# Performance work log

Hardware: AMD Instinct MI355X
Metric: run time of the kernel (lower is better)

Reference implementation:

```python
import jax, jax.numpy as jnp
import numpy as np

N, E, C, RB, H = 10000, 160000, 64, 8, 64
AVG_NEIGH = 16.0


def _sph(v):
    # component-normalized real spherical harmonics l=1,2,3 of unit vectors v [E,3]
    x, y, z = v[..., 0], v[..., 1], v[..., 2]
    s3, s5, s15 = 3.0 ** 0.5, 5.0 ** 0.5, 15.0 ** 0.5
    y1 = s3 * jnp.stack([x, y, z], -1)  # [E,3]
    y2 = jnp.stack([
        s15 * x * y,
        s15 * y * z,
        0.5 * s5 * (3.0 * z * z - 1.0),
        s15 * x * z,
        0.5 * s15 * (x * x - y * y),
    ], -1)  # [E,5]
    c1 = (35.0 / 8.0) ** 0.5
    c2 = 105.0 ** 0.5
    c3 = (21.0 / 8.0) ** 0.5
    c4 = (7.0 ** 0.5) / 2.0
    y3 = jnp.stack([
        c1 * y * (3.0 * x * x - y * y),
        c2 * x * y * z,
        c3 * y * (5.0 * z * z - 1.0),
        c4 * z * (5.0 * z * z - 3.0),
        c3 * x * (5.0 * z * z - 1.0),
        0.5 * c2 * z * (x * x - y * y),
        c1 * x * (x * x - y * y),
    ], -1)  # [E,7]
    return y1, y2, y3


def setup_inputs() -> dict:
    key = jax.random.key(0)
    ks = jax.random.split(key, 12)
    inp = {
        'vectors': jax.random.normal(ks[0], (E, 3), jnp.float32),
        'node_feats': jax.random.normal(ks[1], (N, C), jnp.float32),
        'radial_embedding': jax.random.normal(ks[2], (E, RB), jnp.float32),
        'W_up': jax.random.normal(ks[3], (C, C), jnp.float32) / np.sqrt(C),
        'mlp_w1': jax.random.normal(ks[4], (RB, H), jnp.float32) / np.sqrt(RB),
        'mlp_w2': jax.random.normal(ks[5], (H, H), jnp.float32) / np.sqrt(H),
        'mlp_w3': jax.random.normal(ks[6], (H, H), jnp.float32) / np.sqrt(H),
        'mlp_w4': jax.random.normal(ks[7], (H, 4 * C), jnp.float32) / np.sqrt(H),
        'W_down': jax.random.normal(ks[8], (4, C, C), jnp.float32) / np.sqrt(C),
        'senders': jax.random.randint(ks[9], (E,), 0, N, jnp.int32),
        'receivers': jax.random.randint(ks[10], (E,), 0, N, jnp.int32),
    }
    return inp


def reference(vectors, node_feats, radial_embedding, W_up, mlp_w1, mlp_w2, mlp_w3, mlp_w4, W_down, senders, receivers):
    n = node_feats.shape[0]
    # linear_up (scalars: plain channel mixing)
    x = node_feats @ W_up                                   # [N,C]
    sf = x[senders]                                         # [E,C] gather
    u = vectors / (jnp.linalg.norm(vectors, axis=-1, keepdims=True) + 1e-12)
    y1, y2, y3 = _sph(u)
    # radial MLP -> per-irrep mixing weights [E, 4C]
    h = jax.nn.silu(radial_embedding @ mlp_w1)
    h = jax.nn.silu(h @ mlp_w2)
    h = jax.nn.silu(h @ mlp_w3)
    mix = h @ mlp_w4
    m0, m1, m2, m3 = jnp.split(mix, 4, axis=-1)             # each [E,C]
    # tensor product of Cx0e with Y_l -> Cx(l), scaled by radial mix
    msg0 = sf * m0                                          # [E,C]
    msg1 = (sf * m1)[:, :, None] * y1[:, None, :]           # [E,C,3]
    msg2 = (sf * m2)[:, :, None] * y2[:, None, :]           # [E,C,5]
    msg3 = (sf * m3)[:, :, None] * y3[:, None, :]           # [E,C,7]
    inv = 1.0 / jnp.sqrt(jnp.asarray(AVG_NEIGH, msg0.dtype))
    seg = lambda m: jax.ops.segment_sum(m, receivers, num_segments=n) * inv
    o0, o1, o2, o3 = seg(msg0), seg(msg1), seg(msg2), seg(msg3)
    # linear_down: per-l channel mixing
    o0 = o0 @ W_down[0]
    o1 = jnp.einsum('ncm,cd->ndm', o1, W_down[1])
    o2 = jnp.einsum('ncm,cd->ndm', o2, W_down[2])
    o3 = jnp.einsum('ncm,cd->ndm', o3, W_down[3])
    return jnp.concatenate([o0, o1.reshape(n, -1), o2.reshape(n, -1), o3.reshape(n, -1)], axis=-1)  # [N, 16C]
```

## Files before the change

kernel.cpp:

```cpp
#include <hip/hip_runtime.h>
#include <math.h>

#define CC 64
typedef _Float16 f16;
typedef _Float16 half8_t __attribute__((ext_vector_type(8)));
typedef float f32x4 __attribute__((ext_vector_type(4)));

__device__ __forceinline__ float silu_f(float v) {
    return v / (1.0f + __expf(-v));
}

__global__ void k_up(const float* __restrict__ nf, const float* __restrict__ Wup,
                     float* __restrict__ x, int N) {
    int tid = blockIdx.x * blockDim.x + threadIdx.x;
    if (tid >= N * CC) return;
    int n = tid >> 6;
    int j = tid & 63;
    const float* nfr = nf + (size_t)n * CC;
    float acc = 0.f;
#pragma unroll
    for (int k = 0; k < CC; ++k) acc += nfr[k] * Wup[k * CC + j];
    x[tid] = acc;
}

__global__ void k_hist(const int* __restrict__ rcv, int* __restrict__ cnt, int E) {
    int e = blockIdx.x * blockDim.x + threadIdx.x;
    if (e < E) atomicAdd(&cnt[rcv[e]], 1);
}

__global__ __launch_bounds__(1024) void k_scan(const int* __restrict__ cnt,
        int* __restrict__ off, int* __restrict__ cur, int N) {
    __shared__ int wsum[16];
    int t = threadIdx.x;
    int wave = t >> 6, lane = t & 63;
    int per = (N + 1023) >> 10;
    int i0 = t * per;
    int s = 0;
    for (int j = 0; j < per; ++j) {
        int i = i0 + j;
        if (i < N) s += cnt[i];
    }
    int sc = s;
#pragma unroll
    for (int d = 1; d < 64; d <<= 1) {
        int u = __shfl_up(sc, d, 64);
        if (lane >= d) sc += u;
    }
    if (lane == 63) wsum[wave] = sc;
    __syncthreads();
    if (wave == 0) {
        int v = (lane < 16) ? wsum[lane] : 0;
        int s2 = v;
#pragma unroll
        for (int d = 1; d < 16; d <<= 1) {
            int u = __shfl_up(s2, d, 64);
            if (lane >= d) s2 += u;
        }
        if (lane < 16) wsum[lane] = s2;
    }
    __syncthreads();
    int base = ((wave > 0) ? wsum[wave - 1] : 0) + (sc - s);
    int run = base;
    for (int j = 0; j < per; ++j) {
        int i = i0 + j;
        if (i < N) { off[i] = run; cur[i] = run; run += cnt[i]; }
    }
    if (t == 1023) off[N] = run;
}

__global__ void k_fill(const int* __restrict__ rcv, const int* __restrict__ snd,
                       const float* __restrict__ vec, int* __restrict__ cur,
                       int* __restrict__ eid, int* __restrict__ sndp,
                       float* __restrict__ yb, int E) {
    int e = blockIdx.x * blockDim.x + threadIdx.x;
    if (e >= E) return;
    int p = atomicAdd(&cur[rcv[e]], 1);
    eid[p] = e;
    sndp[p] = snd[e];

    float vx = vec[(size_t)e * 3 + 0];
    float vy = vec[(size_t)e * 3 + 1];
    float vz = vec[(size_t)e * 3 + 2];
    float nrm = sqrtf(vx * vx + vy * vy + vz * vz) + 1e-12f;
    float rinv = 1.0f / nrm;
    float ux = vx * rinv, uy = vy * rinv, uz = vz * rinv;

    const float s3 = 1.7320508075688772f;
    const float s5 = 2.2360679774997896f;
    const float s15 = 3.8729833462074170f;
    const float c1 = 2.0916500663351889f;
    const float c2 = 10.246950765959598f;
    const float c3 = 1.6201851746019651f;
    const float c4 = 1.3228756555322954f;

    float zz = uz * uz, xx = ux * ux, yy = uy * uy;
    float4 r0 = {1.0f, s3 * ux, s3 * uy, s3 * uz};
    float4 r1 = {s15 * ux * uy, s15 * uy * uz, 0.5f * s5 * (3.f * zz - 1.f),
                 s15 * ux * uz};
    float4 r2 = {0.5f * s15 * (xx - yy), c1 * uy * (3.f * xx - yy),
                 c2 * ux * uy * uz, c3 * uy * (5.f * zz - 1.f)};
    float4 r3 = {c4 * uz * (5.f * zz - 3.f), c3 * ux * (5.f * zz - 1.f),
                 0.5f * c2 * uz * (xx - yy), c1 * ux * (xx - yy)};
    float* yr = yb + (size_t)p * 16;
    *(float4*)(yr + 0)  = r0;
    *(float4*)(yr + 4)  = r1;
    *(float4*)(yr + 8)  = r2;
    *(float4*)(yr + 12) = r3;
}

__global__ __launch_bounds__(256) void k_mlp(const float* __restrict__ rad,
        const float* __restrict__ w1, const float* __restrict__ w2,
        const float* __restrict__ w3, const float* __restrict__ w4,
        const int* __restrict__ eid, f16* __restrict__ mixp, int E) {
    __shared__ f16 wB[64][72];
    __shared__ f16 wC[64][72];
    __shared__ f16 act[128][72];

    int t = threadIdx.x;
    int e0 = blockIdx.x * 128;
    int lane = t & 63;
    int wid = t >> 6;

    {
        int n = t & 63;
        int k0 = t >> 6;
        for (int k = k0; k < 64; k += 4) {
            wB[n][k] = (f16)w2[k * 64 + n];
            wC[n][k] = (f16)w3[k * 64 + n];
        }
    }

    {
        int i = t & 127;
        int jh = (t >> 7) * 32;
        int ci = e0 + i;
        float r[8];
        if (ci < E) {
            int e = eid[ci];
#pragma unroll
            for (int k = 0; k < 8; ++k) r[k] = rad[(size_t)e * 8 + k];
        } else {
#pragma unroll
            for (int k = 0; k < 8; ++k) r[k] = 0.f;
        }
        float a[32];
#pragma unroll
        for (int j = 0; j < 32; ++j) a[j] = 0.f;
#pragma unroll
        for (int k = 0; k < 8; ++k) {
            float rv = r[k];
#pragma unroll
            for (int j = 0; j < 32; ++j) a[j] += rv * w1[k * 64 + jh + j];
        }
#pragma unroll
        for (int jj = 0; jj < 32; jj += 8) {
            half8_t h;
#pragma unroll
            for (int u = 0; u < 8; ++u) h[u] = (f16)silu_f(a[jj + u]);
            *(half8_t*)&act[i][jh + jj] = h;
        }
    }
    __syncthreads();

    int m0 = wid * 32;
    int fm = lane & 15;
    int q  = lane >> 4;

    auto loadA = [&](int mbase, int kc) -> half8_t {
        return *(const half8_t*)&act[mbase + fm][kc + q * 8];
    };

    {
        half8_t a00 = loadA(m0, 0),      a01 = loadA(m0, 32);
        half8_t a10 = loadA(m0 + 16, 0), a11 = loadA(m0 + 16, 32);
#pragma unroll
        for (int nt = 0; nt < 4; ++nt) {
            half8_t b0 = *(const half8_t*)&wB[nt * 16 + fm][q * 8];
            half8_t b1 = *(const half8_t*)&wB[nt * 16 + fm][32 + q * 8];
            f32x4 c0 = {0.f, 0.f, 0.f, 0.f};
            c0 = __builtin_amdgcn_mfma_f32_16x16x32_f16(a00, b0, c0, 0, 0, 0);
            c0 = __builtin_amdgcn_mfma_f32_16x16x32_f16(a01, b1, c0, 0, 0, 0);
            f32x4 c1 = {0.f, 0.f, 0.f, 0.f};
            c1 = __builtin_amdgcn_mfma_f32_16x16x32_f16(a10, b0, c1, 0, 0, 0);
            c1 = __builtin_amdgcn_mfma_f32_16x16x32_f16(a11, b1, c1, 0, 0, 0);
#pragma unroll
            for (int r = 0; r < 4; ++r) {
                act[m0 + q * 4 + r][nt * 16 + fm]      = (f16)silu_f(c0[r]);
                act[m0 + 16 + q * 4 + r][nt * 16 + fm] = (f16)silu_f(c1[r]);
            }
        }
    }

    {
        half8_t a00 = loadA(m0, 0),      a01 = loadA(m0, 32);
        half8_t a10 = loadA(m0 + 16, 0), a11 = loadA(m0 + 16, 32);
#pragma unroll
        for (int nt = 0; nt < 4; ++nt) {
            half8_t b0 = *(const half8_t*)&wC[nt * 16 + fm][q * 8];
            half8_t b1 = *(const half8_t*)&wC[nt * 16 + fm][32 + q * 8];
            f32x4 c0 = {0.f, 0.f, 0.f, 0.f};
            c0 = __builtin_amdgcn_mfma_f32_16x16x32_f16(a00, b0, c0, 0, 0, 0);
            c0 = __builtin_amdgcn_mfma_f32_16x16x32_f16(a01, b1, c0, 0, 0, 0);
            f32x4 c1 = {0.f, 0.f, 0.f, 0.f};
            c1 = __builtin_amdgcn_mfma_f32_16x16x32_f16(a10, b0, c1, 0, 0, 0);
            c1 = __builtin_amdgcn_mfma_f32_16x16x32_f16(a11, b1, c1, 0, 0, 0);
#pragma unroll
            for (int r = 0; r < 4; ++r) {
                act[m0 + q * 4 + r][nt * 16 + fm]      = (f16)silu_f(c0[r]);
                act[m0 + 16 + q * 4 + r][nt * 16 + fm] = (f16)silu_f(c1[r]);
            }
        }
    }

    half8_t A00 = loadA(m0, 0),      A01 = loadA(m0, 32);
    half8_t A10 = loadA(m0 + 16, 0), A11 = loadA(m0 + 16, 32);

    auto do_l = [&](int l, f16 (*w)[72]) {
#pragma unroll
        for (int nt = 0; nt < 4; ++nt) {
            half8_t b0 = *(const half8_t*)&w[nt * 16 + fm][q * 8];
            half8_t b1 = *(const half8_t*)&w[nt * 16 + fm][32 + q * 8];
            f32x4 c0 = {0.f, 0.f, 0.f, 0.f};
            c0 = __builtin_amdgcn_mfma_f32_16x16x32_f16(A00, b0, c0, 0, 0, 0);
            c0 = __builtin_amdgcn_mfma_f32_16x16x32_f16(A01, b1, c0, 0, 0, 0);
            f32x4 c1 = {0.f, 0.f, 0.f, 0.f};
            c1 = __builtin_amdgcn_mfma_f32_16x16x32_f16(A10, b0, c1, 0, 0, 0);
            c1 = __builtin_amdgcn_mfma_f32_16x16x32_f16(A11, b1, c1, 0, 0, 0);
#pragma unroll
            for (int r = 0; r < 4; ++r) {
                act[m0 + q * 4 + r][nt * 16 + fm]      = (f16)c0[r];
                act[m0 + 16 + q * 4 + r][nt * 16 + fm] = (f16)c1[r];
            }
        }
#pragma unroll
        for (int it = 0; it < 4; ++it) {
            int row = (lane >> 3) + it * 8;
            int ci = e0 + m0 + row;
            if (ci < E) {
                half8_t v = *(const half8_t*)&act[m0 + row][(lane & 7) * 8];
                *(half8_t*)&mixp[(size_t)ci * 256 + l * 64 + (lane & 7) * 8] = v;
            }
        }
    };

    __syncthreads();
    {
        int n = t & 63;
        int k0 = t >> 6;
        for (int k = k0; k < 64; k += 4) {
            wB[n][k] = (f16)w4[k * 256 + n];
            wC[n][k] = (f16)w4[k * 256 + 64 + n];
        }
    }
    __syncthreads();
    do_l(0, wB);
    do_l(1, wC);
    __syncthreads();
    {
        int n = t & 63;
        int k0 = t >> 6;
        for (int k = k0; k < 64; k += 4) {
            wB[n][k] = (f16)w4[k * 256 + 128 + n];
            wC[n][k] = (f16)w4[k * 256 + 192 + n];
        }
    }
    __syncthreads();
    do_l(2, wB);
    do_l(3, wC);
}

__global__ __launch_bounds__(256) void k_gather(const float* __restrict__ x,
        const f16* __restrict__ mixp, const float* __restrict__ yb,
        const int* __restrict__ sndp, const int* __restrict__ off,
        const float* __restrict__ Wd, float* __restrict__ out, int N) {
    __shared__ float sbuf[4][64 * 20];
    int wv = threadIdx.x >> 6;
    int lane = threadIdx.x & 63;
    int n = blockIdx.x * 4 + wv;
    if (n >= N) return;

    float o[16];
#pragma unroll
    for (int i = 0; i < 16; ++i) o[i] = 0.f;

    auto process = [&](int i) {
        int s = sndp[i];
        const float* yr = yb + (size_t)i * 16;
        float4 A = *(const float4*)(yr + 0);
        float4 B = *(const float4*)(yr + 4);
        float4 Cv = *(const float4*)(yr + 8);
        float4 D = *(const float4*)(yr + 12);
        float sf = x[(size_t)s * 64 + lane];
        const f16* mr = mixp + (size_t)i * 256;
        float t0 = sf * (float)mr[lane];
        float t1 = sf * (float)mr[64 + lane];
        float t2 = sf * (float)mr[128 + lane];
        float t3 = sf * (float)mr[192 + lane];
        o[0]  += t0;
        o[1]  += t1 * A.y;
        o[2]  += t1 * A.z;
        o[3]  += t1 * A.w;
        o[4]  += t2 * B.x;
        o[5]  += t2 * B.y;
        o[6]  += t2 * B.z;
        o[7]  += t2 * B.w;
        o[8]  += t2 * Cv.x;
        o[9]  += t3 * Cv.y;
        o[10] += t3 * Cv.z;
        o[11] += t3 * Cv.w;
        o[12] += t3 * D.x;
        o[13] += t3 * D.y;
        o[14] += t3 * D.z;
        o[15] += t3 * D.w;
    };

    int beg = off[n], end = off[n + 1];
    int i = beg;
    for (; i + 1 < end; i += 2) { process(i); process(i + 1); }
    if (i < end) process(i);

    float* sw = sbuf[wv];
#pragma unroll
    for (int a = 0; a < 4; ++a) {
        f32x4 vq = {o[4 * a + 0], o[4 * a + 1], o[4 * a + 2], o[4 * a + 3]};
        *(f32x4*)&sw[lane * 20 + 4 * a] = vq;
    }

    f32x4 dA = {0.f, 0.f, 0.f, 0.f}, dB = dA, dC = dA, dD = dA;
#pragma unroll 1
    for (int c = 0; c < 64; ++c) {
        f32x4 q0 = *(const f32x4*)&sw[c * 20 + 0];
        f32x4 q1 = *(const f32x4*)&sw[c * 20 + 4];
        f32x4 q2 = *(const f32x4*)&sw[c * 20 + 8];
        f32x4 q3 = *(const f32x4*)&sw[c * 20 + 12];
        float w0  = Wd[c * 64 + lane];
        float w1r = Wd[4096 + c * 64 + lane];
        float w2r = Wd[8192 + c * 64 + lane];
        float w3r = Wd[12288 + c * 64 + lane];
        f32x4 wA = {w0, w1r, w1r, w1r};
        f32x4 wC4 = {w2r, w3r, w3r, w3r};
        dA += q0 * wA;
        dB += q1 * w2r;
        dC += q2 * wC4;
        dD += q3 * w3r;
    }

    float* outr = out + (size_t)n * 1024;
    outr[lane] = 0.25f * dA[0];
#pragma unroll
    for (int m = 0; m < 3; ++m) outr[64 + lane * 3 + m] = 0.25f * dA[1 + m];
    outr[256 + lane * 5 + 0] = 0.25f * dB[0];
    outr[256 + lane * 5 + 1] = 0.25f * dB[1];
    outr[256 + lane * 5 + 2] = 0.25f * dB[2];
    outr[256 + lane * 5 + 3] = 0.25f * dB[3];
    outr[256 + lane * 5 + 4] = 0.25f * dC[0];
    outr[576 + lane * 7 + 0] = 0.25f * dC[1];
    outr[576 + lane * 7 + 1] = 0.25f * dC[2];
    outr[576 + lane * 7 + 2] = 0.25f * dC[3];
    outr[576 + lane * 7 + 3] = 0.25f * dD[0];
    outr[576 + lane * 7 + 4] = 0.25f * dD[1];
    outr[576 + lane * 7 + 5] = 0.25f * dD[2];
    outr[576 + lane * 7 + 6] = 0.25f * dD[3];
}

extern "C" void kernel_launch(void* const* d_in, const int* in_sizes, int n_in,
                              void* d_out, int out_size, void* d_ws, size_t ws_size,
                              hipStream_t stream) {
    const float* vectors    = (const float*)d_in[0];
    const float* node_feats = (const float*)d_in[1];
    const float* radial     = (const float*)d_in[2];
    const float* W_up       = (const float*)d_in[3];
    const float* w1         = (const float*)d_in[4];
    const float* w2         = (const float*)d_in[5];
    const float* w3         = (const float*)d_in[6];
    const float* w4         = (const float*)d_in[7];
    const float* Wd         = (const float*)d_in[8];
    const int*   snd        = (const int*)d_in[9];
    const int*   rcv        = (const int*)d_in[10];
    float* out = (float*)d_out;

    int E = in_sizes[9];
    int N = in_sizes[1] / CC;

    float* ws   = (float*)d_ws;
    float* x    = ws;
    float* yb   = x + (size_t)N * 64;
    f16*   mixp = (f16*)(yb + (size_t)E * 16);
    int*   cnt  = (int*)((char*)mixp + (size_t)E * 256 * sizeof(f16));
    int*   off  = cnt + N;
    int*   cur  = off + (N + 1);
    int*   eid  = cur + N;
    int*   sndp = eid + E;

    hipMemsetAsync(cnt, 0, (size_t)N * sizeof(int), stream);

    k_up<<<(N * CC + 255) / 256, 256, 0, stream>>>(node_feats, W_up, x, N);
    k_hist<<<(E + 255) / 256, 256, 0, stream>>>(rcv, cnt, E);
    k_scan<<<1, 1024, 0, stream>>>(cnt, off, cur, N);
    k_fill<<<(E + 255) / 256, 256, 0, stream>>>(rcv, snd, vectors, cur, eid, sndp, yb, E);
    k_mlp<<<(E + 127) / 128, 256, 0, stream>>>(radial, w1, w2, w3, w4, eid, mixp, E);
    k_gather<<<(N + 3) / 4, 256, 0, stream>>>(x, mixp, yb, sndp, off, Wd, out, N);
}
```

Measured before the change: 248.1 us.

## Pretranspose MLP weights to fp16 once and read MFMA B operands from global

A new small kernel converts and transposes the four radial-MLP weight matrices to fp16 once per call, writing them into the workspace. The MLP kernel no longer stages weights through shared memory with strided per-block conversion and barriers; it loads B fragments directly from global memory (served from cache). The first layer is also moved from scalar FMAs to a zero-padded MFMA. This drops shared-memory usage and syncthreads, which may raise occupancy, but adds a kernel launch and relies on cache hits for the repeated global weight reads.

```diff
diff --git a/kernel.cpp b/kernel.cpp
--- a/kernel.cpp
+++ b/kernel.cpp
@@ -21,6 +21,27 @@
 #pragma unroll
     for (int k = 0; k < CC; ++k) acc += nfr[k] * Wup[k * CC + j];
     x[tid] = acc;
+}
+
+__global__ void k_wt(const float* __restrict__ w1, const float* __restrict__ w2,
+                     const float* __restrict__ w3, const float* __restrict__ w4,
+                     f16* __restrict__ wT1, f16* __restrict__ wT2,
+                     f16* __restrict__ wT3, f16* __restrict__ wT4) {
+    int i = blockIdx.x * 256 + threadIdx.x;
+    if (i < 2048) {
+        int n = i >> 5, k = i & 31;
+        wT1[i] = (k < 8) ? (f16)w1[k * 64 + n] : (f16)0.f;
+    } else if (i < 6144) {
+        int j = i - 2048; int n = j >> 6, k = j & 63;
+        wT2[j] = (f16)w2[k * 64 + n];
+    } else if (i < 10240) {
+        int j = i - 6144; int n = j >> 6, k = j & 63;
+        wT3[j] = (f16)w3[k * 64 + n];
+    } else if (i < 26624) {
+        int j = i - 10240; int l = j >> 12; int r = j & 4095;
+        int n = r >> 6, k = r & 63;
+        wT4[j] = (f16)w4[k * 256 + l * 64 + n];
+    }
 }
 
 __global__ void k_hist(const int* __restrict__ rcv, int* __restrict__ cnt, int E) {
@@ -109,74 +130,69 @@
 }
 
 __global__ __launch_bounds__(256) void k_mlp(const float* __restrict__ rad,
-        const float* __restrict__ w1, const float* __restrict__ w2,
-        const float* __restrict__ w3, const float* __restrict__ w4,
+        const f16* __restrict__ wT1, const f16* __restrict__ wT2,
+        const f16* __restrict__ wT3, const f16* __restrict__ wT4,
         const int* __restrict__ eid, f16* __restrict__ mixp, int E) {
-    __shared__ f16 wB[64][72];
-    __shared__ f16 wC[64][72];
     __shared__ f16 act[128][72];
 
     int t = threadIdx.x;
     int e0 = blockIdx.x * 128;
     int lane = t & 63;
     int wid = t >> 6;
-
-    {
-        int n = t & 63;
-        int k0 = t >> 6;
-        for (int k = k0; k < 64; k += 4) {
-            wB[n][k] = (f16)w2[k * 64 + n];
-            wC[n][k] = (f16)w3[k * 64 + n];
-        }
-    }
-
-    {
-        int i = t & 127;
-        int jh = (t >> 7) * 32;
-        int ci = e0 + i;
-        float r[8];
-        if (ci < E) {
-            int e = eid[ci];
-#pragma unroll
-            for (int k = 0; k < 8; ++k) r[k] = rad[(size_t)e * 8 + k];
-        } else {
-#pragma unroll
-            for (int k = 0; k < 8; ++k) r[k] = 0.f;
-        }
-        float a[32];
-#pragma unroll
-        for (int j = 0; j < 32; ++j) a[j] = 0.f;
-#pragma unroll
-        for (int k = 0; k < 8; ++k) {
-            float rv = r[k];
-#pragma unroll
-            for (int j = 0; j < 32; ++j) a[j] += rv * w1[k * 64 + jh + j];
-        }
-#pragma unroll
-        for (int jj = 0; jj < 32; jj += 8) {
-            half8_t h;
-#pragma unroll
-            for (int u = 0; u < 8; ++u) h[u] = (f16)silu_f(a[jj + u]);
-            *(half8_t*)&act[i][jh + jj] = h;
-        }
-    }
-    __syncthreads();
-
     int m0 = wid * 32;
     int fm = lane & 15;
     int q  = lane >> 4;
 
+    const half8_t hz = {0, 0, 0, 0, 0, 0, 0, 0};
+
+    half8_t a0 = hz, a1 = hz;
+    if (q == 0) {
+        int ci0 = e0 + m0 + fm;
+        if (ci0 < E) {
+            int e = eid[ci0];
+            float4 p0 = *(const float4*)(rad + (size_t)e * 8);
+            float4 p1 = *(const float4*)(rad + (size_t)e * 8 + 4);
+            a0 = (half8_t){(f16)p0.x, (f16)p0.y, (f16)p0.z, (f16)p0.w,
+                           (f16)p1.x, (f16)p1.y, (f16)p1.z, (f16)p1.w};
+        }
+        int ci1 = e0 + m0 + 16 + fm;
+        if (ci1 < E) {
+            int e = eid[ci1];
+            float4 p0 = *(const float4*)(rad + (size_t)e * 8);
+            float4 p1 = *(const float4*)(rad + (size_t)e * 8 + 4);
+            a1 = (half8_t){(f16)p0.x, (f16)p0.y, (f16)p0.z, (f16)p0.w,
+                           (f16)p1.x, (f16)p1.y, (f16)p1.z, (f16)p1.w};
+        }
+    }
+#pragma unroll
+    for (int nt = 0; nt < 4; ++nt) {
+        half8_t b = *(const half8_t*)(wT1 + ((nt * 16 + fm) << 5) + q * 8);
+        f32x4 c0 = {0.f, 0.f, 0.f, 0.f};
+        c0 = __builtin_amdgcn_mfma_f32_16x16x32_f16(a0, b, c0, 0, 0, 0);
+        f32x4 c1 = {0.f, 0.f, 0.f, 0.f};
+        c1 = __builtin_amdgcn_mfma_f32_16x16x32_f16(a1, b, c1, 0, 0, 0);
+#pragma unroll
+        for (int r = 0; r < 4; ++r) {
+            act[m0 + q * 4 + r][nt * 16 + fm]      = (f16)silu_f(c0[r]);
+            act[m0 + 16 + q * 4 + r][nt * 16 + fm] = (f16)silu_f(c1[r]);
+        }
+    }
+
     auto loadA = [&](int mbase, int kc) -> half8_t {
         return *(const half8_t*)&act[mbase + fm][kc + q * 8];
     };
 
-    {
+    const f16* wts[2] = {wT2, wT3};
+#pragma unroll
+    for (int L = 0; L < 2; ++L) {
+        const f16* wT = wts[L];
         half8_t a00 = loadA(m0, 0),      a01 = loadA(m0, 32);
         half8_t a10 = loadA(m0 + 16, 0), a11 = loadA(m0 + 16, 32);
 #pragma unroll
         for (int nt = 0; nt < 4; ++nt) {
-            half8_t b0 = *(const half8_t*)&wB[nt * 16 + fm][q * 8];
-            half8_t b1 = *(const half8_t*)&wB[nt * 16 + fm][32 + q * 8];
+            const f16* wr = wT + ((nt * 16 + fm) << 6);
+            half8_t b0 = *(const half8_t*)(wr + q * 8);
+            half8_t b1 = *(const half8_t*)(wr + 32 + q * 8);
             f32x4 c0 = {0.f, 0.f, 0.f, 0.f};
             c0 = __builtin_amdgcn_mfma_f32_16x16x32_f16(a00, b0, c0, 0, 0, 0);
             c0 = __builtin_amdgcn_mfma_f32_16x16x32_f16(a01, b1, c0, 0, 0, 0);
@@ -191,35 +207,17 @@
         }
     }
 
-    {
-        half8_t a00 = loadA(m0, 0),      a01 = loadA(m0, 32);
-        half8_t a10 = loadA(m0 + 16, 0), a11 = loadA(m0 + 16, 32);
-#pragma unroll
-        for (int nt = 0; nt < 4; ++nt) {
-            half8_t b0 = *(const half8_t*)&wC[nt * 16 + fm][q * 8];
-            half8_t b1 = *(const half8_t*)&wC[nt * 16 + fm][32 + q * 8];
-            f32x4 c0 = {0.f, 0.f, 0.f, 0.f};
-            c0 = __builtin_amdgcn_mfma_f32_16x16x32_f16(a00, b0, c0, 0, 0, 0);
-            c0 = __builtin_amdgcn_mfma_f32_16x16x32_f16(a01, b1, c0, 0, 0, 0);
-            f32x4 c1 = {0.f, 0.f, 0.f, 0.f};
-            c1 = __builtin_amdgcn_mfma_f32_16x16x32_f16(a10, b0, c1, 0, 0, 0);
-            c1 = __builtin_amdgcn_mfma_f32_16x16x32_f16(a11, b1, c1, 0, 0, 0);
-#pragma unroll
-            for (int r = 0; r < 4; ++r) {
-                act[m0 + q * 4 + r][nt * 16 + fm]      = (f16)silu_f(c0[r]);
-                act[m0 + 16 + q * 4 + r][nt * 16 + fm] = (f16)silu_f(c1[r]);
-            }
-        }
-    }
-
     half8_t A00 = loadA(m0, 0),      A01 = loadA(m0, 32);
     half8_t A10 = loadA(m0 + 16, 0), A11 = loadA(m0 + 16, 32);
 
-    auto do_l = [&](int l, f16 (*w)[72]) {
+#pragma unroll
+    for (int l = 0; l < 4; ++l) {
+        const f16* wT = wT4 + (l << 12);
 #pragma unroll
         for (int nt = 0; nt < 4; ++nt) {
-            half8_t b0 = *(const half8_t*)&w[nt * 16 + fm][q * 8];
-            half8_t b1 = *(const half8_t*)&w[nt * 16 + fm][32 + q * 8];
+            const f16* wr = wT + ((nt * 16 + fm) << 6);
+            half8_t b0 = *(const half8_t*)(wr + q * 8);
+            half8_t b1 = *(const half8_t*)(wr + 32 + q * 8);
             f32x4 c0 = {0.f, 0.f, 0.f, 0.f};
             c0 = __builtin_amdgcn_mfma_f32_16x16x32_f16(A00, b0, c0, 0, 0, 0);
             c0 = __builtin_amdgcn_mfma_f32_16x16x32_f16(A01, b1, c0, 0, 0, 0);
@@ -241,32 +239,7 @@
                 *(half8_t*)&mixp[(size_t)ci * 256 + l * 64 + (lane & 7) * 8] = v;
             }
         }
-    };
-
-    __syncthreads();
-    {
-        int n = t & 63;
-        int k0 = t >> 6;
-        for (int k = k0; k < 64; k += 4) {
-            wB[n][k] = (f16)w4[k * 256 + n];
-            wC[n][k] = (f16)w4[k * 256 + 64 + n];
-        }
-    }
-    __syncthreads();
-    do_l(0, wB);
-    do_l(1, wC);
-    __syncthreads();
-    {
-        int n = t & 63;
-        int k0 = t >> 6;
-        for (int k = k0; k < 64; k += 4) {
-            wB[n][k] = (f16)w4[k * 256 + 128 + n];
-            wC[n][k] = (f16)w4[k * 256 + 192 + n];
-        }
-    }
-    __syncthreads();
-    do_l(2, wB);
-    do_l(3, wC);
+    }
 }
 
 __global__ __launch_bounds__(256) void k_gather(const float* __restrict__ x,
@@ -382,11 +355,14 @@
     int E = in_sizes[9];
     int N = in_sizes[1] / CC;
 
-    float* ws   = (float*)d_ws;
-    float* x    = ws;
+    f16*   wT1  = (f16*)d_ws;
+    f16*   wT2  = wT1 + 2048;
+    f16*   wT3  = wT2 + 4096;
+    f16*   wT4  = wT3 + 4096;
+    float* x    = (float*)(wT4 + 16384);
     float* yb   = x + (size_t)N * 64;
     f16*   mixp = (f16*)(yb + (size_t)E * 16);
-    int*   cnt  = (int*)((char*)mixp + (size_t)E * 256 * sizeof(f16));
+    int*   cnt  = (int*)(mixp + (size_t)E * 256);
     int*   off  = cnt + N;
     int*   cur  = off + (N + 1);
     int*   eid  = cur + N;
@@ -394,10 +370,11 @@
 
     hipMemsetAsync(cnt, 0, (size_t)N * sizeof(int), stream);
 
+    k_wt<<<(26624 + 255) / 256, 256, 0, stream>>>(w1, w2, w3, w4, wT1, wT2, wT3, wT4);
     k_up<<<(N * CC + 255) / 256, 256, 0, stream>>>(node_feats, W_up, x, N);
     k_hist<<<(E + 255) / 256, 256, 0, stream>>>(rcv, cnt, E);
     k_scan<<<1, 1024, 0, stream>>>(cnt, off, cur, N);
     k_fill<<<(E + 255) / 256, 256, 0, stream>>>(rcv, snd, vectors, cur, eid, sndp, yb, E);
-    k_mlp<<<(E + 127) / 128, 256, 0, stream>>>(radial, w1, w2, w3, w4, eid, mixp, E);
+    k_mlp<<<(E + 127) / 128, 256, 0, stream>>>(radial, wT1, wT2, wT3, wT4, eid, mixp, E);
     k_gather<<<(N + 3) / 4, 256, 0, stream>>>(x, mixp, yb, sndp, off, Wd, out, N);
 }
```

New measurement: 246.9 us. Within noise of the previous version (-0.5%).
